# Kernel optimization log

Hardware: AMD Instinct MI355X
Metric: run time of the kernel (lower is better)

The kernel has to match this reference:

```python
import jax, jax.numpy as jnp
import numpy as np

N, E, E_LG = 20000, 320000, 600000
F_NODE, F_EDGE, HID, OUT = 256, 64, 256, 40


def _seg_softmax(e, idx, n):
    m = jax.ops.segment_max(e, idx, num_segments=n)
    ex = jnp.exp(e - m[idx])
    s = jax.ops.segment_sum(ex, idx, num_segments=n)
    return ex / (s[idx] + 1e-16)


def _gat(xf, edge_index, W, a_s, a_d, b, n):
    # PyG-style single-head GATConv with self-loops
    h = xf @ W                                   # [n, HID]
    loops = jnp.arange(n, dtype=edge_index.dtype)
    src = jnp.concatenate([edge_index[0], loops])
    dst = jnp.concatenate([edge_index[1], loops])
    e = jax.nn.leaky_relu((h @ a_s)[src] + (h @ a_d)[dst], 0.2)
    alpha = _seg_softmax(e, dst, n)
    return jax.ops.segment_sum(alpha[:, None] * h[src], dst, num_segments=n) + b


def _sage(xf, src, dst, Wr, Wn, b, n):
    # mean-aggregation SAGEConv with root weight
    deg = jnp.clip(jax.ops.segment_sum(jnp.ones(src.shape, xf.dtype), dst, num_segments=n), 1.0)
    mean = jax.ops.segment_sum(xf[src], dst, num_segments=n) / deg[:, None]
    return xf @ Wr + mean @ Wn + b


def setup_inputs() -> dict:
    key = jax.random.key(0)
    ks = jax.random.split(key, 40)
    g = lambda i, shape, fan: jax.random.normal(ks[i], shape, jnp.float32) * np.float32(np.sqrt(2.0 / fan))
    inp = {
        'x': jax.random.normal(ks[0], (N, F_NODE), jnp.float32),
        'et': jax.random.normal(ks[1], (E, F_EDGE), jnp.float32),
        'H': jax.random.randint(ks[2], (2, E), 0, N, jnp.int32),
        'raw_edge_index': jax.random.randint(ks[3], (2, E), 0, N, jnp.int32),
        'lg_edge_index': jax.random.randint(ks[4], (2, E_LG), 0, E, jnp.int32),
        # EdgeGCNV2: GATConv + EdgeToNodeConv + Linear
        'W_gat': g(5, (F_EDGE, HID), F_EDGE), 'a_src': g(6, (HID,), HID), 'a_dst': g(7, (HID,), HID),
        'b_gat': jnp.zeros((HID,), jnp.float32),
        'W_etn': g(8, (HID, HID), HID), 'W_eg': g(9, (HID, HID), HID),
        # edge_aggr SAGE: num_layers-1 = 2 layers
        'Wr_e1': g(10, (HID, HID), HID), 'Wn_e1': g(11, (HID, HID), HID), 'b_e1': jnp.zeros((HID,), jnp.float32),
        'Wr_e2': g(12, (HID, HID), HID), 'Wn_e2': g(13, (HID, HID), HID), 'b_e2': jnp.zeros((HID,), jnp.float32),
        # attr_node SAGE: num_layers = 3 layers
        'Wr_n1': g(14, (F_NODE, HID), F_NODE), 'Wn_n1': g(15, (F_NODE, HID), F_NODE), 'b_n1': jnp.zeros((HID,), jnp.float32),
        'Wr_n2': g(16, (HID, HID), HID), 'Wn_n2': g(17, (HID, HID), HID), 'b_n2': jnp.zeros((HID,), jnp.float32),
        'Wr_n3': g(18, (HID, HID), HID), 'Wn_n3': g(19, (HID, HID), HID), 'b_n3': jnp.zeros((HID,), jnp.float32),
        # MixAttention
        'Wq': g(20, (HID, HID), HID), 'Wk': g(21, (HID, HID), HID), 'Wv': g(22, (HID, HID), HID),
        # final linear (glorot, no bias)
        'W_out': g(23, (HID, OUT), HID),
    }
    return inp


def reference(x, et, H, raw_edge_index, lg_edge_index,
              W_gat, a_src, a_dst, b_gat, W_etn, W_eg,
              Wr_e1, Wn_e1, b_e1, Wr_e2, Wn_e2, b_e2,
              Wr_n1, Wn_n1, b_n1, Wr_n2, Wn_n2, b_n2, Wr_n3, Wn_n3, b_n3,
              Wq, Wk, Wv, W_out):
    src, dst = raw_edge_index[0], raw_edge_index[1]

    # ---- EdgeGCNV2: GAT over line graph, then edge->node incidence aggregation ----
    gat_out = _gat(et, lg_edge_index, W_gat, a_src, a_dst, b_gat, E)   # [E, HID]
    he = gat_out @ W_etn
    acc = (jax.ops.segment_sum(he, H[0], num_segments=N)
           + jax.ops.segment_sum(he, H[1], num_segments=N))            # [N, HID]
    ones_e = jnp.ones((E,), he.dtype)
    deg = (jax.ops.segment_sum(ones_e, H[0], num_segments=N)
           + jax.ops.segment_sum(ones_e, H[1], num_segments=N))
    etn = acc / jnp.clip(deg, 1.0)[:, None]
    edge_repr = jax.nn.leaky_relu(etn, 0.2) @ W_eg                     # [N, HID]

    # ---- edge_aggr SAGE (2 layers, relu between) ----
    h = jax.nn.relu(_sage(edge_repr, src, dst, Wr_e1, Wn_e1, b_e1, N))
    aggr_edge = _sage(h, src, dst, Wr_e2, Wn_e2, b_e2, N)

    # ---- attr_node SAGE (3 layers) ----
    h = jax.nn.relu(_sage(x, src, dst, Wr_n1, Wn_n1, b_n1, N))
    h = jax.nn.relu(_sage(h, src, dst, Wr_n2, Wn_n2, b_n2, N))
    node_repr = _sage(h, src, dst, Wr_n3, Wn_n3, b_n3, N)

    # ---- MixAttention: node queries attend over neighbor edge-derived keys/values ----
    q, k, v = node_repr @ Wq, aggr_edge @ Wk, aggr_edge @ Wv
    sc = jnp.sum(q[dst] * k[src], axis=-1) * np.float32(1.0 / np.sqrt(HID))
    alpha = _seg_softmax(sc, dst, N)
    mixed = node_repr + jax.ops.segment_sum(alpha[:, None] * v[src], dst, num_segments=N)

    logits = mixed @ W_out
    return jax.nn.log_softmax(logits, axis=1)
```

## Files before the change

kernel.cpp:

```cpp
#include <hip/hip_runtime.h>
#include <math.h>

#define NN   20000
#define EE   320000
#define ELG  600000
#define FE   64
#define HD   256
#define FOUT 40
#define LOG2E 1.44269504f
#define NTOTC (NN + EE + NN)
#define NIDX  (EE + ELG + 2 * EE)

typedef __attribute__((ext_vector_type(8))) short bf16x8;
typedef __attribute__((ext_vector_type(4))) float f32x4;

__device__ __forceinline__ float leaky02(float x) { return x > 0.f ? x : 0.2f * x; }

__device__ __forceinline__ unsigned short bf16rne(float f) {
    unsigned int u = __float_as_uint(f);
    u = (u + 0x7FFFu + ((u >> 16) & 1u)) >> 16;
    return (unsigned short)u;
}
__device__ __forceinline__ float bflo(unsigned int u) { return __uint_as_float(u << 16); }
__device__ __forceinline__ float bfhi(unsigned int u) { return __uint_as_float(u & 0xffff0000u); }
__device__ __forceinline__ unsigned int bfpack(float a, float b) {
    return (unsigned int)bf16rne(a) | ((unsigned int)bf16rne(b) << 16);
}

__global__ void zero_i32(int* __restrict__ p, int n) {
    int i = blockIdx.x * 256 + threadIdx.x;
    if (i < n) p[i] = 0;
}
__global__ void conv_bf16(const float* __restrict__ in, unsigned int* __restrict__ out, int n2) {
    int i = blockIdx.x * 256 + threadIdx.x;
    if (i < n2) { float2 v = ((const float2*)in)[i]; out[i] = bfpack(v.x, v.y); }
}

__global__ void count_all(const int* __restrict__ dstN, const int* __restrict__ lgd,
                          const int* __restrict__ Hm, int* __restrict__ cntAll) {
    int i = blockIdx.x * 256 + threadIdx.x;
    if (i >= NIDX) return;
    if (i < EE) atomicAdd(&cntAll[dstN[i]], 1);
    else if (i < EE + ELG) atomicAdd(&cntAll[NN + lgd[i - EE]], 1);
    else atomicAdd(&cntAll[NN + EE + Hm[i - EE - ELG]], 1);
}

__global__ void scan_pass1(const int* __restrict__ in, int* __restrict__ bsum, int n) {
    __shared__ int sm[256];
    int base = blockIdx.x * 1024, t = threadIdx.x;
    int s = 0;
#pragma unroll
    for (int j = 0; j < 4; ++j) { int i = base + t * 4 + j; s += (i < n) ? in[i] : 0; }
    sm[t] = s; __syncthreads();
    for (int o = 128; o > 0; o >>= 1) { if (t < o) sm[t] += sm[t + o]; __syncthreads(); }
    if (t == 0) bsum[blockIdx.x] = sm[0];
}
__global__ void scan_pass2(int* __restrict__ bsum, int nb) {
    __shared__ int sm[1024];
    int t = threadIdx.x;
    for (int i = t; i < nb; i += 256) sm[i] = bsum[i];
    __syncthreads();
    if (t == 0) { int run = 0; for (int i = 0; i < nb; ++i) { int v = sm[i]; sm[i] = run; run += v; } }
    __syncthreads();
    for (int i = t; i < nb; i += 256) bsum[i] = sm[i];
}
__global__ void scan_pass3(const int* __restrict__ in, const int* __restrict__ boff,
                           int* __restrict__ out, int n) {
    __shared__ int tsum[256];
    int base = blockIdx.x * 1024, t = threadIdx.x;
    int v[4];
#pragma unroll
    for (int j = 0; j < 4; ++j) { int i = base + t * 4 + j; v[j] = (i < n) ? in[i] : 0; }
    int loc = v[0] + v[1] + v[2] + v[3];
    tsum[t] = loc; __syncthreads();
    for (int o = 1; o < 256; o <<= 1) {
        int x = (t >= o) ? tsum[t - o] : 0;
        __syncthreads();
        tsum[t] += x;
        __syncthreads();
    }
    int off = boff[blockIdx.x] + (tsum[t] - loc);
    int run = 0;
#pragma unroll
    for (int j = 0; j < 4; ++j) { int i = base + t * 4 + j; if (i < n) out[i] = off + run; run += v[j]; }
}

__global__ void rebase_all(const int* __restrict__ scanAll,
                           int* __restrict__ rowptrD, int* __restrict__ cursD,
                           int* __restrict__ rowptrLG, int* __restrict__ cursLG,
                           int* __restrict__ rowptrH, int* __restrict__ cursH) {
    int i = blockIdx.x * 256 + threadIdx.x;
    if (i == 0) { rowptrD[NN] = EE; rowptrLG[EE] = ELG; rowptrH[NN] = 2 * EE; }
    if (i >= NTOTC) return;
    if (i < NN) { int v = scanAll[i]; rowptrD[i] = v; cursD[i] = v; }
    else if (i < NN + EE) { int v = scanAll[i] - EE; rowptrLG[i - NN] = v; cursLG[i - NN] = v; }
    else { int v = scanAll[i] - (EE + ELG); rowptrH[i - NN - EE] = v; cursH[i - NN - EE] = v; }
}

__global__ void place_all(const int* __restrict__ srcN, const int* __restrict__ dstN,
                          const int* __restrict__ lgs, const int* __restrict__ lgd,
                          const int* __restrict__ Hm,
                          int* __restrict__ cursD, int* __restrict__ cursLG, int* __restrict__ cursH,
                          int* __restrict__ adjS, int* __restrict__ adjLG, int* __restrict__ adjH) {
    int i = blockIdx.x * 256 + threadIdx.x;
    if (i >= NIDX) return;
    if (i < EE) {
        int pos = atomicAdd(&cursD[dstN[i]], 1);
        adjS[pos] = srcN[i];
    } else if (i < EE + ELG) {
        int j = i - EE;
        int pos = atomicAdd(&cursLG[lgd[j]], 1);
        adjLG[pos] = lgs[j];
    } else {
        int j = i - EE - ELG;
        int pos = atomicAdd(&cursH[Hm[j]], 1);
        adjH[pos] = (j < EE) ? j : j - EE;
    }
}

struct Ptr14 { const float* p[14]; };
__global__ void wtrans14(Ptr14 srcs, unsigned short* __restrict__ dst) {
    int m = blockIdx.x >> 6;
    int tile = blockIdx.x & 63;
    const float* src = srcs.p[m];
    unsigned short* out = dst + (size_t)m * 65536;
    int kb = (tile >> 3) * 32, nb = (tile & 7) * 32;
    __shared__ float sm[32][33];
    int t = threadIdx.x;
#pragma unroll
    for (int i = 0; i < 4; ++i) {
        int e = t + i * 256; int r = e >> 5, c = e & 31;
        sm[r][c] = src[(kb + r) * 256 + nb + c];
    }
    __syncthreads();
#pragma unroll
    for (int i = 0; i < 4; ++i) {
        int e = t + i * 256; int nr = e >> 5, kc = e & 31;
        out[(size_t)(nb + nr) * 256 + kb + kc] = bf16rne(sm[kc][nr]);
    }
}
__global__ void wtrans_one(const float* __restrict__ src, unsigned short* __restrict__ dst,
                           int K, int N) {
    int tilesN = N >> 5;
    int kb = (blockIdx.x / tilesN) * 32, nb = (blockIdx.x % tilesN) * 32;
    __shared__ float sm[32][33];
    int t = threadIdx.x;
#pragma unroll
    for (int i = 0; i < 4; ++i) {
        int e = t + i * 256; int r = e >> 5, c = e & 31;
        sm[r][c] = src[(kb + r) * N + nb + c];
    }
    __syncthreads();
#pragma unroll
    for (int i = 0; i < 4; ++i) {
        int e = t + i * 256; int nr = e >> 5, kc = e & 31;
        dst[(size_t)(nb + nr) * K + kb + kc] = bf16rne(sm[kc][nr]);
    }
}

__global__ __launch_bounds__(256)
void gemm_bf16(const unsigned short* __restrict__ A1, const unsigned short* __restrict__ A2,
               const unsigned short* __restrict__ W1, const unsigned short* __restrict__ W2,
               const float* __restrict__ bias, const float* __restrict__ degmask,
               unsigned short* __restrict__ C, int M, int K1, int flags) {
    __shared__ unsigned short As[128][40];
    __shared__ unsigned short Bs[64][40];
    int tid = threadIdx.x;
    int w = tid >> 6, l = tid & 63;
    int wr = w >> 1, wc = w & 1;
    int brow = blockIdx.y * 128, bcol = blockIdx.x * 64;
    int Ktot = K1 + (A2 ? 256 : 0);
    f32x4 acc[4][2] = {};
    for (int k0 = 0; k0 < Ktot; k0 += 32) {
        const unsigned short* Ap; const unsigned short* Wp; int kk, Klen;
        if (k0 < K1) { Ap = A1; Wp = W1; kk = k0; Klen = K1; }
        else         { Ap = A2; Wp = W2; kk = k0 - K1; Klen = 256; }
#pragma unroll
        for (int i = 0; i < 4; ++i) {
            int q = tid + i * 256;
            int r = q >> 3, kb = (q & 7) * 4;
            int gr = brow + r;
            ushort4 u;
            if (gr < M) u = *(const ushort4*)(Ap + (size_t)gr * Klen + kk + kb);
            else { u.x = 0; u.y = 0; u.z = 0; u.w = 0; }
            *(ushort4*)(&As[r][kb]) = u;
        }
#pragma unroll
        for (int i = 0; i < 2; ++i) {
            int q = tid + i * 256;
            int n = q >> 3, kb = (q & 7) * 4;
            *(ushort4*)(&Bs[n][kb]) = *(const ushort4*)(Wp + (size_t)(bcol + n) * Klen + kk + kb);
        }
        __syncthreads();
        bf16x8 af[4], bfr[2];
#pragma unroll
        for (int fr = 0; fr < 4; ++fr)
            af[fr] = *(const bf16x8*)(&As[wr * 64 + fr * 16 + (l & 15)][(l >> 4) * 8]);
#pragma unroll
        for (int fc = 0; fc < 2; ++fc)
            bfr[fc] = *(const bf16x8*)(&Bs[wc * 32 + fc * 16 + (l & 15)][(l >> 4) * 8]);
#pragma unroll
        for (int fr = 0; fr < 4; ++fr)
#pragma unroll
            for (int fc = 0; fc < 2; ++fc)
                acc[fr][fc] = __builtin_amdgcn_mfma_f32_16x16x32_bf16(af[fr], bfr[fc], acc[fr][fc], 0, 0, 0);
        __syncthreads();
    }
#pragma unroll
    for (int fr = 0; fr < 4; ++fr) {
#pragma unroll
        for (int fc = 0; fc < 2; ++fc) {
            int col = bcol + wc * 32 + fc * 16 + (l & 15);
#pragma unroll
            for (int i = 0; i < 4; ++i) {
                int row = brow + wr * 64 + fr * 16 + (l >> 4) * 4 + i;
                if (row >= M) continue;
                float v = acc[fr][fc][i];
                if (bias) v += bias[col];
                if (flags & 1) v = fmaxf(v, 0.f);
                if (flags & 4) { v = (degmask[row] > 0.f) ? v : 0.f; v = leaky02(v); }
                C[(size_t)row * 256 + col] = bf16rne(v);
            }
        }
    }
}

__global__ __launch_bounds__(256)
void gemm_bf16_tri(const unsigned short* __restrict__ A0, const unsigned short* __restrict__ W0,
                   unsigned short* __restrict__ C0,
                   const unsigned short* __restrict__ A1, const unsigned short* __restrict__ W1,
                   unsigned short* __restrict__ C1,
                   const unsigned short* __restrict__ A2, const unsigned short* __restrict__ W2,
                   unsigned short* __restrict__ C2, int M) {
    __shared__ unsigned short As[128][40];
    __shared__ unsigned short Bs[64][40];
    int sel = blockIdx.x >> 2;
    const unsigned short* A = (sel == 0) ? A0 : (sel == 1) ? A1 : A2;
    const unsigned short* W = (sel == 0) ? W0 : (sel == 1) ? W1 : W2;
    unsigned short* C = (sel == 0) ? C0 : (sel == 1) ? C1 : C2;
    int tid = threadIdx.x;
    int w = tid >> 6, l = tid & 63;
    int wr = w >> 1, wc = w & 1;
    int brow = blockIdx.y * 128, bcol = (blockIdx.x & 3) * 64;
    f32x4 acc[4][2] = {};
    for (int k0 = 0; k0 < 256; k0 += 32) {
#pragma unroll
        for (int i = 0; i < 4; ++i) {
            int q = tid + i * 256;
            int r = q >> 3, kb = (q & 7) * 4;
            int gr = brow + r;
            ushort4 u;
            if (gr < M) u = *(const ushort4*)(A + (size_t)gr * 256 + k0 + kb);
            else { u.x = 0; u.y = 0; u.z = 0; u.w = 0; }
            *(ushort4*)(&As[r][kb]) = u;
        }
#pragma unroll
        for (int i = 0; i < 2; ++i) {
            int q = tid + i * 256;
            int n = q >> 3, kb = (q & 7) * 4;
            *(ushort4*)(&Bs[n][kb]) = *(const ushort4*)(W + (size_t)(bcol + n) * 256 + k0 + kb);
        }
        __syncthreads();
        bf16x8 af[4], bfr[2];
#pragma unroll
        for (int fr = 0; fr < 4; ++fr)
            af[fr] = *(const bf16x8*)(&As[wr * 64 + fr * 16 + (l & 15)][(l >> 4) * 8]);
#pragma unroll
        for (int fc = 0; fc < 2; ++fc)
            bfr[fc] = *(const bf16x8*)(&Bs[wc * 32 + fc * 16 + (l & 15)][(l >> 4) * 8]);
#pragma unroll
        for (int fr = 0; fr < 4; ++fr)
#pragma unroll
            for (int fc = 0; fc < 2; ++fc)
                acc[fr][fc] = __builtin_amdgcn_mfma_f32_16x16x32_bf16(af[fr], bfr[fc], acc[fr][fc], 0, 0, 0);
        __syncthreads();
    }
#pragma unroll
    for (int fr = 0; fr < 4; ++fr) {
#pragma unroll
        for (int fc = 0; fc < 2; ++fc) {
            int col = bcol + wc * 32 + fc * 16 + (l & 15);
#pragma unroll
            for (int i = 0; i < 4; ++i) {
                int row = brow + wr * 64 + fr * 16 + (l >> 4) * 4 + i;
                if (row >= M) continue;
                C[(size_t)row * 256 + col] = bf16rne(acc[fr][fc][i]);
            }
        }
    }
}

__global__ __launch_bounds__(256)
void gemm_f32(const float* __restrict__ A, const float* __restrict__ B,
              float* __restrict__ C, int M, int N, int K) {
    const int BM = 64, BN = 64, BK = 16;
    __shared__ float As[BK][BM + 1];
    __shared__ float Bs[BK][BN + 1];
    int tid = threadIdx.x;
    int tr = tid >> 4, tc = tid & 15;
    int brow = blockIdx.y * BM, bcol = blockIdx.x * BN;
    float acc[4][4] = {{0.f}};
    for (int k0 = 0; k0 < K; k0 += BK) {
#pragma unroll
        for (int i = 0; i < 4; ++i) {
            int e = tid + i * 256;
            int r = e >> 4, c = e & 15;
            int gr = brow + r, gc = k0 + c;
            As[c][r] = (gr < M && gc < K) ? A[(long)gr * K + gc] : 0.f;
        }
#pragma unroll
        for (int i = 0; i < 4; ++i) {
            int e = tid + i * 256;
            int r = e >> 6, c = e & 63;
            int gr = k0 + r, gc = bcol + c;
            Bs[r][c] = (gr < K && gc < N) ? B[(long)gr * N + gc] : 0.f;
        }
        __syncthreads();
#pragma unroll
        for (int k = 0; k < BK; ++k) {
            float ra[4], rb[4];
#pragma unroll
            for (int i = 0; i < 4; ++i) ra[i] = As[k][tr * 4 + i];
#pragma unroll
            for (int j = 0; j < 4; ++j) rb[j] = Bs[k][tc * 4 + j];
#pragma unroll
            for (int i = 0; i < 4; ++i)
#pragma unroll
                for (int j = 0; j < 4; ++j) acc[i][j] += ra[i] * rb[j];
        }
        __syncthreads();
    }
#pragma unroll
    for (int i = 0; i < 4; ++i) {
        int gr = brow + tr * 4 + i;
        if (gr >= M) continue;
#pragma unroll
        for (int j = 0; j < 4; ++j) {
            int gc = bcol + tc * 4 + j;
            if (gc < N) C[(long)gr * N + gc] = acc[i][j];
        }
    }
}

__global__ __launch_bounds__(256)
void gemm_out_lsm(const float* __restrict__ A, const float* __restrict__ B,
                  float* __restrict__ out, int M) {
    const int BK = 16;
    __shared__ float As[BK][65];
    __shared__ float Bs[BK][65];
    __shared__ float tile[64][41];
    __shared__ float lsb[64];
    int tid = threadIdx.x;
    int tr = tid >> 4, tc = tid & 15;
    int brow = blockIdx.y * 64;
    float acc[4][4] = {{0.f}};
    for (int k0 = 0; k0 < 256; k0 += BK) {
#pragma unroll
        for (int i = 0; i < 4; ++i) {
            int e = tid + i * 256;
            int r = e >> 4, c = e & 15;
            int gr = brow + r;
            As[c][r] = (gr < M) ? A[(long)gr * 256 + k0 + c] : 0.f;
        }
#pragma unroll
        for (int i = 0; i < 4; ++i) {
            int e = tid + i * 256;
            int r = e >> 6, c = e & 63;
            Bs[r][c] = (c < FOUT) ? B[(long)(k0 + r) * FOUT + c] : 0.f;
        }
        __syncthreads();
#pragma unroll
        for (int k = 0; k < BK; ++k) {
            float ra[4], rb[4];
#pragma unroll
            for (int i = 0; i < 4; ++i) ra[i] = As[k][tr * 4 + i];
#pragma unroll
            for (int j = 0; j < 4; ++j) rb[j] = Bs[k][tc * 4 + j];
#pragma unroll
            for (int i = 0; i < 4; ++i)
#pragma unroll
                for (int j = 0; j < 4; ++j) acc[i][j] += ra[i] * rb[j];
        }
        __syncthreads();
    }
#pragma unroll
    for (int i = 0; i < 4; ++i)
#pragma unroll
        for (int j = 0; j < 4; ++j) {
            int gc = tc * 4 + j;
            if (gc < FOUT) tile[tr * 4 + i][gc] = acc[i][j];
        }
    __syncthreads();
    if (tid < 64) {
        int gr = brow + tid;
        float mx = -INFINITY;
        if (gr < M) {
            for (int c = 0; c < FOUT; ++c) mx = fmaxf(mx, tile[tid][c]);
            float s = 0.f;
            for (int c = 0; c < FOUT; ++c) s += __expf(tile[tid][c] - mx);
            lsb[tid] = mx + logf(s);
        }
    }
    __syncthreads();
#pragma unroll
    for (int i = 0; i < 4; ++i) {
        int r = tr * 4 + i;
        int gr = brow + r;
        if (gr >= M) continue;
#pragma unroll
        for (int j = 0; j < 4; ++j) {
            int gc = tc * 4 + j;
            if (gc < FOUT) out[(long)gr * FOUT + gc] = tile[r][gc] - lsb[r];
        }
    }
}

__global__ void gat_prep(const float* __restrict__ W, const float* __restrict__ as_,
                         const float* __restrict__ ad_, const float* __restrict__ b_gat,
                         const float* __restrict__ W_etn,
                         float* __restrict__ asv, float* __restrict__ adv, float* __restrict__ b2) {
    int t = threadIdx.x;
    if (blockIdx.x == FE) {
        float s = 0.f;
        for (int i = 0; i < HD; ++i) s += b_gat[i] * W_etn[i * HD + t];
        b2[t] = s;
        return;
    }
    __shared__ float sm[256];
    int i = blockIdx.x;
    float w = W[i * HD + t];
    sm[t] = w * as_[t];
    __syncthreads();
    for (int o = 128; o > 0; o >>= 1) { if (t < o) sm[t] += sm[t + o]; __syncthreads(); }
    if (t == 0) asv[i] = sm[0];
    __syncthreads();
    sm[t] = w * ad_[t];
    __syncthreads();
    for (int o = 128; o > 0; o >>= 1) { if (t < o) sm[t] += sm[t + o]; __syncthreads(); }
    if (t == 0) adv[i] = sm[0];
}

__global__ void edge_scores_conv(const float* __restrict__ et, const float* __restrict__ asv,
                                 const float* __restrict__ adv, float* __restrict__ es,
                                 float* __restrict__ ed, unsigned short* __restrict__ et_bf) {
    int e = blockIdx.x * 4 + (threadIdx.x >> 6);
    int l = threadIdx.x & 63;
    float x = et[(long)e * FE + l];
    et_bf[(long)e * FE + l] = bf16rne(x);
    float vs = x * asv[l];
    float vd = x * adv[l];
    for (int o = 32; o > 0; o >>= 1) { vs += __shfl_down(vs, o); vd += __shfl_down(vd, o); }
    if (l == 0) { es[e] = vs; ed[e] = vd; }
}

__global__ void seg_alpha(const int* __restrict__ rowptr, const int* __restrict__ adj,
                          const float* __restrict__ es, const float* __restrict__ ed,
                          float* __restrict__ alphaS, float* __restrict__ alphaL) {
    int d = blockIdx.x * 256 + threadIdx.x;
    if (d >= EE) return;
    int b = rowptr[d], e_ = rowptr[d + 1];
    float edd = ed[d];
    float selfsc = leaky02(es[d] + edd);
    float m = selfsc;
    for (int i = b; i < e_; ++i) m = fmaxf(m, leaky02(es[adj[i]] + edd));
    float s = __expf(selfsc - m);
    for (int i = b; i < e_; ++i) s += __expf(leaky02(es[adj[i]] + edd) - m);
    float inv = 1.f / (s + 1e-16f);
    alphaS[d] = __expf(selfsc - m) * inv;
    for (int i = b; i < e_; ++i) alphaL[i] = __expf(leaky02(es[adj[i]] + edd) - m) * inv;
}

__global__ void gat_gather3(const int* __restrict__ rowptr, const int* __restrict__ adj,
                            const float* __restrict__ alphaS, const float* __restrict__ alphaL,
                            const unsigned short* __restrict__ et_bf,
                            unsigned short* __restrict__ agg_et) {
    int d = blockIdx.x * 32 + (threadIdx.x >> 3);
    int hl = threadIdx.x & 7;
    if (d >= EE) return;
    int b = rowptr[d], e_ = rowptr[d + 1];
    const uint4* etu = (const uint4*)et_bf;
    float al = alphaS[d];
    uint4 u = etu[(size_t)d * 8 + hl];
    float a0 = al * bflo(u.x), a1 = al * bfhi(u.x), a2 = al * bflo(u.y), a3 = al * bfhi(u.y);
    float a4 = al * bflo(u.z), a5 = al * bfhi(u.z), a6 = al * bflo(u.w), a7 = al * bfhi(u.w);
    for (int i = b; i < e_; ++i) {
        al = alphaL[i];
        u = etu[(size_t)adj[i] * 8 + hl];
        a0 += al * bflo(u.x); a1 += al * bfhi(u.x); a2 += al * bflo(u.y); a3 += al * bfhi(u.y);
        a4 += al * bflo(u.z); a5 += al * bfhi(u.z); a6 += al * bflo(u.w); a7 += al * bfhi(u.w);
    }
    uint4 o;
    o.x = bfpack(a0, a1); o.y = bfpack(a2, a3); o.z = bfpack(a4, a5); o.w = bfpack(a6, a7);
    ((uint4*)agg_et)[(size_t)d * 8 + hl] = o;
}

__global__ void etn_gather2(const int* __restrict__ rowptr, const int* __restrict__ adj,
                            const unsigned short* __restrict__ agg_et,
                            unsigned short* __restrict__ agg2, float* __restrict__ degE) {
    int base = (blockIdx.x * 4 + (threadIdx.x >> 6)) * 4;
    int lane = threadIdx.x & 63;
    int q = lane >> 4, hl = lane & 15;
    int n = base + q;
    if (n >= NN) return;
    int b = rowptr[n], e_ = rowptr[n + 1];
    const uint2* au = (const uint2*)agg_et;
    float a0 = 0.f, a1 = 0.f, a2 = 0.f, a3 = 0.f;
    for (int i = b; i < e_; ++i) {
        uint2 u = au[(size_t)adj[i] * 16 + hl];
        a0 += bflo(u.x); a1 += bfhi(u.x); a2 += bflo(u.y); a3 += bfhi(u.y);
    }
    float deg = (float)(e_ - b);
    float inv = 1.f / fmaxf(deg, 1.f);
    uint2 o; o.x = bfpack(a0 * inv, a1 * inv); o.y = bfpack(a2 * inv, a3 * inv);
    ((uint2*)agg2)[(size_t)n * 16 + hl] = o;
    if (hl == 0) degE[n] = deg;
}

__global__ void sage_gather2(const unsigned short* __restrict__ X, const int* __restrict__ rowptr,
                             const int* __restrict__ adjS, unsigned short* __restrict__ mean) {
    int base = (blockIdx.x * 4 + (threadIdx.x >> 6)) * 2;
    int lane = threadIdx.x & 63;
    int half = lane >> 5, hl = lane & 31;
    int n = base + half;
    if (n >= NN) return;
    int b = rowptr[n], e_ = rowptr[n + 1];
    const uint4* Xu = (const uint4*)X;
    float a0 = 0.f, a1 = 0.f, a2 = 0.f, a3 = 0.f, a4 = 0.f, a5 = 0.f, a6 = 0.f, a7 = 0.f;
    for (int i = b; i < e_; ++i) {
        uint4 u = Xu[(size_t)adjS[i] * 32 + hl];
        a0 += bflo(u.x); a1 += bfhi(u.x); a2 += bflo(u.y); a3 += bfhi(u.y);
        a4 += bflo(u.z); a5 += bfhi(u.z); a6 += bflo(u.w); a7 += bfhi(u.w);
    }
    float inv = 1.f / fmaxf((float)(e_ - b), 1.f);
    uint4 o;
    o.x = bfpack(a0 * inv, a1 * inv); o.y = bfpack(a2 * inv, a3 * inv);
    o.z = bfpack(a4 * inv, a5 * inv); o.w = bfpack(a6 * inv, a7 * inv);
    ((uint4*)mean)[(size_t)n * 32 + hl] = o;
}

__global__ void attn_online(const unsigned short* __restrict__ q, const unsigned short* __restrict__ k,
                            const unsigned short* __restrict__ v, const unsigned short* __restrict__ nrep,
                            const int* __restrict__ rowptr, const int* __restrict__ adjS,
                            float* __restrict__ mixed) {
    int n = blockIdx.x * 4 + (threadIdx.x >> 6);
    int lane = threadIdx.x & 63;
    if (n >= NN) return;
    int half = lane >> 5, hl = lane & 31;
    int b = rowptr[n], e_ = rowptr[n + 1];
    const uint4* qu4 = (const uint4*)q;
    const uint4* ku4 = (const uint4*)k;
    const uint4* vu4 = (const uint4*)v;
    const uint4* nu4 = (const uint4*)nrep;
    uint4 nu = nu4[(size_t)n * 32 + hl];
    float nr0 = bflo(nu.x), nr1 = bfhi(nu.x), nr2 = bflo(nu.y), nr3 = bfhi(nu.y);
    float nr4 = bflo(nu.z), nr5 = bfhi(nu.z), nr6 = bflo(nu.w), nr7 = bfhi(nu.w);
    float* mrow = mixed + (size_t)n * HD;
    if (b == e_) {
        if (half == 0) {
            ((float4*)mrow)[2 * hl]     = make_float4(nr0, nr1, nr2, nr3);
            ((float4*)mrow)[2 * hl + 1] = make_float4(nr4, nr5, nr6, nr7);
        }
        return;
    }
    uint4 qv = qu4[(size_t)n * 32 + hl];
    float q0 = bflo(qv.x), q1 = bfhi(qv.x), q2 = bflo(qv.y), q3 = bfhi(qv.y);
    float q4 = bflo(qv.z), q5 = bfhi(qv.z), q6 = bflo(qv.w), q7 = bfhi(qv.w);
    float m = -INFINITY, srun = 0.f;
    float a0 = 0.f, a1 = 0.f, a2 = 0.f, a3 = 0.f, a4 = 0.f, a5 = 0.f, a6 = 0.f, a7 = 0.f;
    for (int i = b + half; i < e_; i += 2) {
        int s = adjS[i];
        uint4 ku = ku4[(size_t)s * 32 + hl];
        float p = q0 * bflo(ku.x) + q1 * bfhi(ku.x) + q2 * bflo(ku.y) + q3 * bfhi(ku.y)
                + q4 * bflo(ku.z) + q5 * bfhi(ku.z) + q6 * bflo(ku.w) + q7 * bfhi(ku.w);
        p += __shfl_xor(p, 1); p += __shfl_xor(p, 2); p += __shfl_xor(p, 4);
        p += __shfl_xor(p, 8); p += __shfl_xor(p, 16);
        p *= 0.0625f;
        uint4 vu = vu4[(size_t)s * 32 + hl];
        float mn = fmaxf(m, p);
        float scale = exp2f((m - mn) * LOG2E);
        float w = exp2f((p - mn) * LOG2E);
        m = mn;
        srun = srun * scale + w;
        a0 = a0 * scale + w * bflo(vu.x); a1 = a1 * scale + w * bfhi(vu.x);
        a2 = a2 * scale + w * bflo(vu.y); a3 = a3 * scale + w * bfhi(vu.y);
        a4 = a4 * scale + w * bflo(vu.z); a5 = a5 * scale + w * bfhi(vu.z);
        a6 = a6 * scale + w * bflo(vu.w); a7 = a7 * scale + w * bfhi(vu.w);
    }
    float mo = __shfl_xor(m, 32);
    float so = __shfl_xor(srun, 32);
    float mn = fmaxf(m, mo);
    float cs = exp2f((m - mn) * LOG2E);
    float co = exp2f((mo - mn) * LOG2E);
    float st = srun * cs + so * co;
    float inv = 1.f / (st + 1e-16f);
    float o0 = (a0 * cs + __shfl_xor(a0, 32) * co) * inv + nr0;
    float o1 = (a1 * cs + __shfl_xor(a1, 32) * co) * inv + nr1;
    float o2 = (a2 * cs + __shfl_xor(a2, 32) * co) * inv + nr2;
    float o3 = (a3 * cs + __shfl_xor(a3, 32) * co) * inv + nr3;
    float o4 = (a4 * cs + __shfl_xor(a4, 32) * co) * inv + nr4;
    float o5 = (a5 * cs + __shfl_xor(a5, 32) * co) * inv + nr5;
    float o6 = (a6 * cs + __shfl_xor(a6, 32) * co) * inv + nr6;
    float o7 = (a7 * cs + __shfl_xor(a7, 32) * co) * inv + nr7;
    if (half == 0) {
        ((float4*)mrow)[2 * hl]     = make_float4(o0, o1, o2, o3);
        ((float4*)mrow)[2 * hl + 1] = make_float4(o4, o5, o6, o7);
    }
}

extern "C" void kernel_launch(void* const* d_in, const int* in_sizes, int n_in,
                              void* d_out, int out_size, void* d_ws, size_t ws_size,
                              hipStream_t stream) {
    (void)in_sizes; (void)n_in; (void)out_size; (void)ws_size;
    const float* x     = (const float*)d_in[0];
    const float* et    = (const float*)d_in[1];
    const int*   Hm    = (const int*)d_in[2];
    const int*   raw   = (const int*)d_in[3];
    const int*   lg    = (const int*)d_in[4];
    const float* W_gat = (const float*)d_in[5];
    const float* a_src = (const float*)d_in[6];
    const float* a_dst = (const float*)d_in[7];
    const float* b_gat = (const float*)d_in[8];
    const float* W_etn = (const float*)d_in[9];
    const float* W_eg  = (const float*)d_in[10];
    const float* Wr_e1 = (const float*)d_in[11];
    const float* Wn_e1 = (const float*)d_in[12];
    const float* b_e1  = (const float*)d_in[13];
    const float* Wr_e2 = (const float*)d_in[14];
    const float* Wn_e2 = (const float*)d_in[15];
    const float* b_e2  = (const float*)d_in[16];
    const float* Wr_n1 = (const float*)d_in[17];
    const float* Wn_n1 = (const float*)d_in[18];
    const float* b_n1  = (const float*)d_in[19];
    const float* Wr_n2 = (const float*)d_in[20];
    const float* Wn_n2 = (const float*)d_in[21];
    const float* b_n2  = (const float*)d_in[22];
    const float* Wr_n3 = (const float*)d_in[23];
    const float* Wn_n3 = (const float*)d_in[24];
    const float* b_n3  = (const float*)d_in[25];
    const float* Wq    = (const float*)d_in[26];
    const float* Wk    = (const float*)d_in[27];
    const float* Wv    = (const float*)d_in[28];
    const float* W_out = (const float*)d_in[29];

    const int* srcN = raw;
    const int* dstN = raw + EE;
    const int* lgs  = lg;
    const int* lgd  = lg + ELG;

    float* ws = (float*)d_ws;
    size_t off = 0;
    auto alloc = [&](size_t n) { float* p = ws + off; off += (n + 63) & ~(size_t)63; return p; };
    auto allocU = [&](size_t nus) { return (unsigned short*)alloc(nus / 2 + 64); };

    unsigned short* et_bf   = allocU((size_t)EE * FE);
    unsigned short* agg_et  = allocU((size_t)EE * FE);
    float* es     = alloc(EE);
    float* ed     = alloc(EE);
    float* alphaS = alloc(EE);
    float* alphaL = alloc(ELG);
    float* Wcomb  = alloc((size_t)FE * HD);
    float* b2     = alloc(HD);
    float* asv    = alloc(FE);
    float* adv    = alloc(FE);
    unsigned short* agg2_bf = allocU((size_t)NN * FE);
    float* degE   = alloc(NN);
    unsigned short* etnL  = allocU((size_t)NN * HD);
    unsigned short* erep  = allocU((size_t)NN * HD);
    unsigned short* meanb = allocU((size_t)NN * HD);
    unsigned short* t1    = allocU((size_t)NN * HD);
    unsigned short* aggr  = allocU((size_t)NN * HD);
    unsigned short* nrep  = allocU((size_t)NN * HD);
    unsigned short* x_bf  = allocU((size_t)NN * HD);
    float* mixed  = alloc((size_t)NN * HD);
    unsigned short* wtb    = allocU((size_t)14 * 65536);
    unsigned short* wcombt = allocU((size_t)HD * FE);
    int* rowptrD  = (int*)alloc(NN + 64);
    int* cursD    = (int*)alloc(NN);
    int* adjS     = (int*)alloc(EE);
    int* rowptrLG = (int*)alloc(EE + 64);
    int* cursLG   = (int*)alloc(EE);
    int* adjLG    = (int*)alloc(ELG);
    int* rowptrH  = (int*)alloc(NN + 64);
    int* cursH    = (int*)alloc(NN);
    int* adjH     = (int*)alloc(2 * EE);
    int* cntAll   = (int*)alloc(NTOTC + 64);
    int* scanAll  = (int*)alloc(NTOTC + 64);
    int* bsum     = (int*)alloc(1024);
    unsigned short* ta = etnL;
    unsigned short* tb = erep;
    unsigned short* qb = agg_et;
    unsigned short* kb = agg_et + (size_t)NN * HD;
    unsigned short* vb = agg_et + (size_t)2 * NN * HD;
    float* outp = (float*)d_out;

    unsigned short* W_eg_t  = wtb + 0 * 65536;
    unsigned short* Wr_e1_t = wtb + 1 * 65536;
    unsigned short* Wn_e1_t = wtb + 2 * 65536;
    unsigned short* Wr_e2_t = wtb + 3 * 65536;
    unsigned short* Wn_e2_t = wtb + 4 * 65536;
    unsigned short* Wr_n1_t = wtb + 5 * 65536;
    unsigned short* Wn_n1_t = wtb + 6 * 65536;
    unsigned short* Wr_n2_t = wtb + 7 * 65536;
    unsigned short* Wn_n2_t = wtb + 8 * 65536;
    unsigned short* Wr_n3_t = wtb + 9 * 65536;
    unsigned short* Wn_n3_t = wtb + 10 * 65536;
    unsigned short* Wq_t    = wtb + 11 * 65536;
    unsigned short* Wk_t    = wtb + 12 * 65536;
    unsigned short* Wv_t    = wtb + 13 * 65536;

    dim3 gB(4, (NN + 127) / 128);

    Ptr14 p14;
    p14.p[0] = W_eg;  p14.p[1] = Wr_e1; p14.p[2] = Wn_e1; p14.p[3] = Wr_e2;
    p14.p[4] = Wn_e2; p14.p[5] = Wr_n1; p14.p[6] = Wn_n1; p14.p[7] = Wr_n2;
    p14.p[8] = Wn_n2; p14.p[9] = Wr_n3; p14.p[10] = Wn_n3; p14.p[11] = Wq;
    p14.p[12] = Wk;   p14.p[13] = Wv;
    wtrans14<<<14 * 64, 256, 0, stream>>>(p14, wtb);
    conv_bf16<<<(NN * HD / 2 + 255) / 256, 256, 0, stream>>>(x, (unsigned int*)x_bf, NN * HD / 2);

    zero_i32<<<(NTOTC + 255) / 256, 256, 0, stream>>>(cntAll, NTOTC);
    count_all<<<(NIDX + 255) / 256, 256, 0, stream>>>(dstN, lgd, Hm, cntAll);
    {
        int nb = (NTOTC + 1023) / 1024;
        scan_pass1<<<nb, 256, 0, stream>>>(cntAll, bsum, NTOTC);
        scan_pass2<<<1, 256, 0, stream>>>(bsum, nb);
        scan_pass3<<<nb, 256, 0, stream>>>(cntAll, bsum, scanAll, NTOTC);
    }
    rebase_all<<<(NTOTC + 255) / 256, 256, 0, stream>>>(scanAll, rowptrD, cursD,
                                                        rowptrLG, cursLG, rowptrH, cursH);
    place_all<<<(NIDX + 255) / 256, 256, 0, stream>>>(srcN, dstN, lgs, lgd, Hm,
                                                      cursD, cursLG, cursH, adjS, adjLG, adjH);

    gemm_f32<<<dim3(4, 1), 256, 0, stream>>>(W_gat, W_etn, Wcomb, FE, HD, HD);
    wtrans_one<<<(FE / 32) * (HD / 32), 256, 0, stream>>>(Wcomb, wcombt, FE, HD);
    gat_prep<<<FE + 1, 256, 0, stream>>>(W_gat, a_src, a_dst, b_gat, W_etn, asv, adv, b2);
    edge_scores_conv<<<EE / 4, 256, 0, stream>>>(et, asv, adv, es, ed, et_bf);
    seg_alpha<<<(EE + 255) / 256, 256, 0, stream>>>(rowptrLG, adjLG, es, ed, alphaS, alphaL);
    gat_gather3<<<EE / 32, 256, 0, stream>>>(rowptrLG, adjLG, alphaS, alphaL, et_bf, agg_et);

    etn_gather2<<<(NN + 15) / 16, 256, 0, stream>>>(rowptrH, adjH, agg_et, agg2_bf, degE);
    gemm_bf16<<<gB, 256, 0, stream>>>(agg2_bf, nullptr, wcombt, nullptr, b2, degE, etnL, NN, FE, 4);
    gemm_bf16<<<gB, 256, 0, stream>>>(etnL, nullptr, W_eg_t, nullptr, nullptr, nullptr, erep, NN, HD, 0);

    sage_gather2<<<(NN + 7) / 8, 256, 0, stream>>>(erep, rowptrD, adjS, meanb);
    gemm_bf16<<<gB, 256, 0, stream>>>(erep, meanb, Wr_e1_t, Wn_e1_t, b_e1, nullptr, t1, NN, HD, 1);
    sage_gather2<<<(NN + 7) / 8, 256, 0, stream>>>(t1, rowptrD, adjS, meanb);
    gemm_bf16<<<gB, 256, 0, stream>>>(t1, meanb, Wr_e2_t, Wn_e2_t, b_e2, nullptr, aggr, NN, HD, 0);

    sage_gather2<<<(NN + 7) / 8, 256, 0, stream>>>(x_bf, rowptrD, adjS, meanb);
    gemm_bf16<<<gB, 256, 0, stream>>>(x_bf, meanb, Wr_n1_t, Wn_n1_t, b_n1, nullptr, ta, NN, HD, 1);
    sage_gather2<<<(NN + 7) / 8, 256, 0, stream>>>(ta, rowptrD, adjS, meanb);
    gemm_bf16<<<gB, 256, 0, stream>>>(ta, meanb, Wr_n2_t, Wn_n2_t, b_n2, nullptr, tb, NN, HD, 1);
    sage_gather2<<<(NN + 7) / 8, 256, 0, stream>>>(tb, rowptrD, adjS, meanb);
    gemm_bf16<<<gB, 256, 0, stream>>>(tb, meanb, Wr_n3_t, Wn_n3_t, b_n3, nullptr, nrep, NN, HD, 0);

    gemm_bf16_tri<<<dim3(12, (NN + 127) / 128), 256, 0, stream>>>(
        nrep, Wq_t, qb, aggr, Wk_t, kb, aggr, Wv_t, vb, NN);
    attn_online<<<(NN + 3) / 4, 256, 0, stream>>>(qb, kb, vb, nrep, rowptrD, adjS, mixed);

    gemm_out_lsm<<<dim3(1, (NN + 63) / 64), 256, 0, stream>>>(mixed, W_out, outp, NN);
}
```

Measured before the change: 883.8 us.

## Range-partition CSR placement and software-prefetch neighbor loads in gather kernels

The CSR placement kernel is split into 8 destination-key ranges per chunk, so each block only does atomics and scatter writes for one range of keys. This is meant to improve locality of the cursor atomics and adjacency writes, at the cost of every block re-reading its input chunk 8 times. The gather loops (GAT, SAGE mean, edge-to-node, attention) now prefetch the next neighbor's row before accumulating the current one, to overlap dependent gather latency. The edge-to-node gather switches to 8 lanes per node with 16-byte loads.

```diff
diff --git a/kernel.cpp b/kernel.cpp
--- a/kernel.cpp
+++ b/kernel.cpp
@@ -10,6 +10,9 @@
 #define LOG2E 1.44269504f
 #define NTOTC (NN + EE + NN)
 #define NIDX  (EE + ELG + 2 * EE)
+#define RD_RANGE  ((NN + 7) / 8)
+#define RLG_RANGE ((EE + 7) / 8)
+#define PCHUNK 4096
 
 typedef __attribute__((ext_vector_type(8))) short bf16x8;
 typedef __attribute__((ext_vector_type(4))) float f32x4;
@@ -97,24 +100,38 @@
     else { int v = scanAll[i] - (EE + ELG); rowptrH[i - NN - EE] = v; cursH[i - NN - EE] = v; }
 }
 
-__global__ void place_all(const int* __restrict__ srcN, const int* __restrict__ dstN,
-                          const int* __restrict__ lgs, const int* __restrict__ lgd,
-                          const int* __restrict__ Hm,
-                          int* __restrict__ cursD, int* __restrict__ cursLG, int* __restrict__ cursH,
-                          int* __restrict__ adjS, int* __restrict__ adjLG, int* __restrict__ adjH) {
-    int i = blockIdx.x * 256 + threadIdx.x;
-    if (i >= NIDX) return;
-    if (i < EE) {
-        int pos = atomicAdd(&cursD[dstN[i]], 1);
-        adjS[pos] = srcN[i];
-    } else if (i < EE + ELG) {
-        int j = i - EE;
-        int pos = atomicAdd(&cursLG[lgd[j]], 1);
-        adjLG[pos] = lgs[j];
-    } else {
-        int j = i - EE - ELG;
-        int pos = atomicAdd(&cursH[Hm[j]], 1);
-        adjH[pos] = (j < EE) ? j : j - EE;
+__global__ void place_ranged(const int* __restrict__ srcN, const int* __restrict__ dstN,
+                             const int* __restrict__ lgs, const int* __restrict__ lgd,
+                             const int* __restrict__ Hm,
+                             int* __restrict__ cursD, int* __restrict__ cursLG, int* __restrict__ cursH,
+                             int* __restrict__ adjS, int* __restrict__ adjLG, int* __restrict__ adjH) {
+    int r = blockIdx.x & 7;
+    int chunk = blockIdx.x >> 3;
+    int beg = chunk * PCHUNK + threadIdx.x;
+    int end = chunk * PCHUNK + PCHUNK;
+    if (end > NIDX) end = NIDX;
+    for (int i = beg; i < end; i += 256) {
+        if (i < EE) {
+            int key = dstN[i];
+            if (key / RD_RANGE == r) {
+                int pos = atomicAdd(&cursD[key], 1);
+                adjS[pos] = srcN[i];
+            }
+        } else if (i < EE + ELG) {
+            int j = i - EE;
+            int key = lgd[j];
+            if (key / RLG_RANGE == r) {
+                int pos = atomicAdd(&cursLG[key], 1);
+                adjLG[pos] = lgs[j];
+            }
+        } else {
+            int j = i - EE - ELG;
+            int key = Hm[j];
+            if (key / RD_RANGE == r) {
+                int pos = atomicAdd(&cursH[key], 1);
+                adjH[pos] = (j < EE) ? j : j - EE;
+            }
+        }
     }
 }
 
@@ -479,40 +496,52 @@
     if (d >= EE) return;
     int b = rowptr[d], e_ = rowptr[d + 1];
     const uint4* etu = (const uint4*)et_bf;
+    int i = b;
+    float aln = 0.f; uint4 un;
+    if (i < e_) { aln = alphaL[i]; un = etu[(size_t)adj[i] * 8 + hl]; }
     float al = alphaS[d];
     uint4 u = etu[(size_t)d * 8 + hl];
     float a0 = al * bflo(u.x), a1 = al * bfhi(u.x), a2 = al * bflo(u.y), a3 = al * bfhi(u.y);
     float a4 = al * bflo(u.z), a5 = al * bfhi(u.z), a6 = al * bflo(u.w), a7 = al * bfhi(u.w);
-    for (int i = b; i < e_; ++i) {
-        al = alphaL[i];
-        u = etu[(size_t)adj[i] * 8 + hl];
-        a0 += al * bflo(u.x); a1 += al * bfhi(u.x); a2 += al * bflo(u.y); a3 += al * bfhi(u.y);
-        a4 += al * bflo(u.z); a5 += al * bfhi(u.z); a6 += al * bflo(u.w); a7 += al * bfhi(u.w);
+    while (i < e_) {
+        float alc = aln; uint4 uc = un;
+        int in = i + 1;
+        if (in < e_) { aln = alphaL[in]; un = etu[(size_t)adj[in] * 8 + hl]; }
+        a0 += alc * bflo(uc.x); a1 += alc * bfhi(uc.x); a2 += alc * bflo(uc.y); a3 += alc * bfhi(uc.y);
+        a4 += alc * bflo(uc.z); a5 += alc * bfhi(uc.z); a6 += alc * bflo(uc.w); a7 += alc * bfhi(uc.w);
+        i = in;
     }
     uint4 o;
     o.x = bfpack(a0, a1); o.y = bfpack(a2, a3); o.z = bfpack(a4, a5); o.w = bfpack(a6, a7);
     ((uint4*)agg_et)[(size_t)d * 8 + hl] = o;
 }
 
-__global__ void etn_gather2(const int* __restrict__ rowptr, const int* __restrict__ adj,
+__global__ void etn_gather3(const int* __restrict__ rowptr, const int* __restrict__ adj,
                             const unsigned short* __restrict__ agg_et,
                             unsigned short* __restrict__ agg2, float* __restrict__ degE) {
-    int base = (blockIdx.x * 4 + (threadIdx.x >> 6)) * 4;
-    int lane = threadIdx.x & 63;
-    int q = lane >> 4, hl = lane & 15;
-    int n = base + q;
+    int n = blockIdx.x * 32 + (threadIdx.x >> 3);
+    int hl = threadIdx.x & 7;
     if (n >= NN) return;
     int b = rowptr[n], e_ = rowptr[n + 1];
-    const uint2* au = (const uint2*)agg_et;
-    float a0 = 0.f, a1 = 0.f, a2 = 0.f, a3 = 0.f;
-    for (int i = b; i < e_; ++i) {
-        uint2 u = au[(size_t)adj[i] * 16 + hl];
-        a0 += bflo(u.x); a1 += bfhi(u.x); a2 += bflo(u.y); a3 += bfhi(u.y);
+    const uint4* au = (const uint4*)agg_et;
+    int i = b;
+    uint4 un;
+    if (i < e_) un = au[(size_t)adj[i] * 8 + hl];
+    float a0 = 0.f, a1 = 0.f, a2 = 0.f, a3 = 0.f, a4 = 0.f, a5 = 0.f, a6 = 0.f, a7 = 0.f;
+    while (i < e_) {
+        uint4 uc = un;
+        int in = i + 1;
+        if (in < e_) un = au[(size_t)adj[in] * 8 + hl];
+        a0 += bflo(uc.x); a1 += bfhi(uc.x); a2 += bflo(uc.y); a3 += bfhi(uc.y);
+        a4 += bflo(uc.z); a5 += bfhi(uc.z); a6 += bflo(uc.w); a7 += bfhi(uc.w);
+        i = in;
     }
     float deg = (float)(e_ - b);
     float inv = 1.f / fmaxf(deg, 1.f);
-    uint2 o; o.x = bfpack(a0 * inv, a1 * inv); o.y = bfpack(a2 * inv, a3 * inv);
-    ((uint2*)agg2)[(size_t)n * 16 + hl] = o;
+    uint4 o;
+    o.x = bfpack(a0 * inv, a1 * inv); o.y = bfpack(a2 * inv, a3 * inv);
+    o.z = bfpack(a4 * inv, a5 * inv); o.w = bfpack(a6 * inv, a7 * inv);
+    ((uint4*)agg2)[(size_t)n * 8 + hl] = o;
     if (hl == 0) degE[n] = deg;
 }
 
@@ -525,11 +554,17 @@
     if (n >= NN) return;
     int b = rowptr[n], e_ = rowptr[n + 1];
     const uint4* Xu = (const uint4*)X;
+    int i = b;
+    uint4 un;
+    if (i < e_) un = Xu[(size_t)adjS[i] * 32 + hl];
     float a0 = 0.f, a1 = 0.f, a2 = 0.f, a3 = 0.f, a4 = 0.f, a5 = 0.f, a6 = 0.f, a7 = 0.f;
-    for (int i = b; i < e_; ++i) {
-        uint4 u = Xu[(size_t)adjS[i] * 32 + hl];
-        a0 += bflo(u.x); a1 += bfhi(u.x); a2 += bflo(u.y); a3 += bfhi(u.y);
-        a4 += bflo(u.z); a5 += bfhi(u.z); a6 += bflo(u.w); a7 += bfhi(u.w);
+    while (i < e_) {
+        uint4 uc = un;
+        int in = i + 1;
+        if (in < e_) un = Xu[(size_t)adjS[in] * 32 + hl];
+        a0 += bflo(uc.x); a1 += bfhi(uc.x); a2 += bflo(uc.y); a3 += bfhi(uc.y);
+        a4 += bflo(uc.z); a5 += bfhi(uc.z); a6 += bflo(uc.w); a7 += bfhi(uc.w);
+        i = in;
     }
     float inv = 1.f / fmaxf((float)(e_ - b), 1.f);
     uint4 o;
@@ -567,15 +602,26 @@
     float q4 = bflo(qv.z), q5 = bfhi(qv.z), q6 = bflo(qv.w), q7 = bfhi(qv.w);
     float m = -INFINITY, srun = 0.f;
     float a0 = 0.f, a1 = 0.f, a2 = 0.f, a3 = 0.f, a4 = 0.f, a5 = 0.f, a6 = 0.f, a7 = 0.f;
-    for (int i = b + half; i < e_; i += 2) {
-        int s = adjS[i];
-        uint4 ku = ku4[(size_t)s * 32 + hl];
+    int i = b + half;
+    uint4 ku, vu;
+    if (i < e_) {
+        int s0 = adjS[i];
+        ku = ku4[(size_t)s0 * 32 + hl];
+        vu = vu4[(size_t)s0 * 32 + hl];
+    }
+    while (i < e_) {
+        int in = i + 2;
+        uint4 kn, vn;
+        if (in < e_) {
+            int s1 = adjS[in];
+            kn = ku4[(size_t)s1 * 32 + hl];
+            vn = vu4[(size_t)s1 * 32 + hl];
+        }
         float p = q0 * bflo(ku.x) + q1 * bfhi(ku.x) + q2 * bflo(ku.y) + q3 * bfhi(ku.y)
                 + q4 * bflo(ku.z) + q5 * bfhi(ku.z) + q6 * bflo(ku.w) + q7 * bfhi(ku.w);
         p += __shfl_xor(p, 1); p += __shfl_xor(p, 2); p += __shfl_xor(p, 4);
         p += __shfl_xor(p, 8); p += __shfl_xor(p, 16);
         p *= 0.0625f;
-        uint4 vu = vu4[(size_t)s * 32 + hl];
         float mn = fmaxf(m, p);
         float scale = exp2f((m - mn) * LOG2E);
         float w = exp2f((p - mn) * LOG2E);
@@ -585,6 +631,7 @@
         a2 = a2 * scale + w * bflo(vu.y); a3 = a3 * scale + w * bfhi(vu.y);
         a4 = a4 * scale + w * bflo(vu.z); a5 = a5 * scale + w * bfhi(vu.z);
         a6 = a6 * scale + w * bflo(vu.w); a7 = a7 * scale + w * bfhi(vu.w);
+        i = in; ku = kn; vu = vn;
     }
     float mo = __shfl_xor(m, 32);
     float so = __shfl_xor(srun, 32);
@@ -728,8 +775,11 @@
     }
     rebase_all<<<(NTOTC + 255) / 256, 256, 0, stream>>>(scanAll, rowptrD, cursD,
                                                         rowptrLG, cursLG, rowptrH, cursH);
-    place_all<<<(NIDX + 255) / 256, 256, 0, stream>>>(srcN, dstN, lgs, lgd, Hm,
-                                                      cursD, cursLG, cursH, adjS, adjLG, adjH);
+    {
+        int nch = (NIDX + PCHUNK - 1) / PCHUNK;
+        place_ranged<<<nch * 8, 256, 0, stream>>>(srcN, dstN, lgs, lgd, Hm,
+                                                  cursD, cursLG, cursH, adjS, adjLG, adjH);
+    }
 
     gemm_f32<<<dim3(4, 1), 256, 0, stream>>>(W_gat, W_etn, Wcomb, FE, HD, HD);
     wtrans_one<<<(FE / 32) * (HD / 32), 256, 0, stream>>>(Wcomb, wcombt, FE, HD);
@@ -738,7 +788,7 @@
     seg_alpha<<<(EE + 255) / 256, 256, 0, stream>>>(rowptrLG, adjLG, es, ed, alphaS, alphaL);
     gat_gather3<<<EE / 32, 256, 0, stream>>>(rowptrLG, adjLG, alphaS, alphaL, et_bf, agg_et);
 
-    etn_gather2<<<(NN + 15) / 16, 256, 0, stream>>>(rowptrH, adjH, agg_et, agg2_bf, degE);
+    etn_gather3<<<(NN + 31) / 32, 256, 0, stream>>>(rowptrH, adjH, agg_et, agg2_bf, degE);
     gemm_bf16<<<gB, 256, 0, stream>>>(agg2_bf, nullptr, wcombt, nullptr, b2, degE, etnL, NN, FE, 4);
     gemm_bf16<<<gB, 256, 0, stream>>>(etnL, nullptr, W_eg_t, nullptr, nullptr, nullptr, erep, NN, HD, 0);
 
```

New measurement: 852.2 us. 1.04x faster.
